# Performance work log

Hardware: AMD Instinct MI355X
Metric: run time of the kernel (lower is better)

## Reference

```python
import jax, jax.numpy as jnp
import numpy as np

B, H, W, C = 32, 56, 56, 256
RATE = 0.5


def setup_inputs() -> dict:
    key = jax.random.key(0)
    k1, k2, k3 = jax.random.split(key, 3)
    x = jax.random.normal(k1, (B, H, W, C), dtype=jnp.float32)
    # One independent spatial permutation per channel (shared across batch),
    # matching tf.random_shuffle of the [H*W, B, 1] reshaped slice.
    perm = jnp.argsort(jax.random.uniform(k2, (C, H * W)), axis=1).astype(jnp.int32)
    # Random subset of floor(rate*C) channels is jumbled (0/1 blend mask),
    # matching tf.scatter_nd over a shuffled channel index vector.
    n_sel = int(np.floor(RATE * C))
    chan_order = jax.random.permutation(k3, C)
    mask = jnp.zeros((C,), dtype=jnp.float32).at[chan_order[:n_sel]].set(1.0)
    return {"x": x, "mask": mask, "perm": perm}


def reference(x, mask, perm) -> jnp.ndarray:
    b, h, w, c = x.shape
    xf = x.reshape(b, h * w, c)                      # [B, HW, C]
    # shuffled[b, p, ch] = xf[b, perm[ch, p], ch]
    shuf = jnp.take_along_axis(xf, perm.T[None, :, :], axis=1)  # [B, HW, C]
    out = shuf * mask + xf * (1.0 - mask)            # per-channel blend
    return out.reshape(b, h, w, c)
```

## Files before the change

kernel.cpp:

```cpp
#include <hip/hip_runtime.h>

#define BATCH 32
#define HW    3136
#define NCH   256
#define CHB   8
#define THREADS 1024

__global__ __launch_bounds__(THREADS) void jumble_staged_kernel(
    const float* __restrict__ x, const float* __restrict__ mask,
    const int* __restrict__ perm, float* __restrict__ out) {
  __shared__ float lds[HW * CHB];

  const unsigned hw_bid = blockIdx.x;
  const unsigned xcd = hw_bid & 7u;
  const unsigned l = hw_bid >> 3;
  const unsigned chblk = l >> 2;
  const unsigned b = 4u * xcd + (l & 3u);
  const unsigned ch0 = chblk * CHB;

  const unsigned t = threadIdx.x;

  const float4* __restrict__ xg4 = (const float4*)(x + (size_t)b * (HW * NCH));
  for (unsigned f = t; f < HW * CHB / 4; f += THREADS) {
    const unsigned p = f >> 1, cq = f & 1u;
    const float4 v = xg4[p * (NCH / 4) + (ch0 / 4) + cq];
    const unsigned cb = cq * 4u;
    lds[(cb + 0) * HW + p] = v.x;
    lds[(cb + 1) * HW + p] = v.y;
    lds[(cb + 2) * HW + p] = v.z;
    lds[(cb + 3) * HW + p] = v.w;
  }

  const unsigned cp = t & 3u;
  const unsigned c0l = 2u * cp;
  const int* __restrict__ permA = perm + (size_t)(ch0 + c0l) * HW;
  const int* __restrict__ permB = perm + (size_t)(ch0 + c0l + 1) * HW;
  const bool m0 = mask[ch0 + c0l] != 0.0f;
  const bool m1 = mask[ch0 + c0l + 1] != 0.0f;

  __syncthreads();

  float2* __restrict__ og2 = (float2*)(out + (size_t)b * (HW * NCH) + ch0);
  for (unsigned f = t; f < HW * CHB / 2; f += THREADS) {
    const unsigned p = f >> 2;
    const int r0 = m0 ? permA[p] : (int)p;
    const int r1 = m1 ? permB[p] : (int)p;
    float2 v;
    v.x = lds[(c0l + 0) * HW + r0];
    v.y = lds[(c0l + 1) * HW + r1];
    og2[p * (NCH / 2) + cp] = v;
  }
}

extern "C" void kernel_launch(void* const* d_in, const int* in_sizes, int n_in,
                              void* d_out, int out_size, void* d_ws, size_t ws_size,
                              hipStream_t stream) {
  const float* x = (const float*)d_in[0];
  const float* mask = (const float*)d_in[1];
  const int* perm = (const int*)d_in[2];
  float* out = (float*)d_out;

  jumble_staged_kernel<<<BATCH * (NCH / CHB), THREADS, 0, stream>>>(
      x, mask, perm, out);
}
```

Measured before the change: 49.26 us.

## Software-pipeline channel units through double-buffered LDS with one block per batch slice

The grid shrinks to 256 blocks, one per batch image and 32-channel slice. Each block walks four 8-channel units, holding the next unit's global loads in registers while the current unit is staged into two LDS buffers and gathered. The aim is to overlap global-load latency with the LDS gather. Output stores also widen to 64 bytes of contiguous channels per pixel. In exchange, each thread carries many float4 registers and there are fewer blocks to hide latency across the GPU.

Result: slower. 112.3 us (+128.0%).

```diff
diff --git a/kernel.cpp b/kernel.cpp
--- a/kernel.cpp
+++ b/kernel.cpp
@@ -1,55 +1,141 @@
 #include <hip/hip_runtime.h>
 
-#define BATCH 32
-#define HW    3136
-#define NCH   256
-#define CHB   8
+#define HW      3136
+#define NCH     256
 #define THREADS 1024
+#define SLOTS   4
+#define TAIL    64
 
-__global__ __launch_bounds__(THREADS) void jumble_staged_kernel(
+__global__ __launch_bounds__(THREADS) void jumble_v5_kernel(
     const float* __restrict__ x, const float* __restrict__ mask,
     const int* __restrict__ perm, float* __restrict__ out) {
-  __shared__ float lds[HW * CHB];
+  __shared__ float bufA[4 * HW];
+  __shared__ float bufB[4 * HW];
 
-  const unsigned hw_bid = blockIdx.x;
-  const unsigned xcd = hw_bid & 7u;
-  const unsigned l = hw_bid >> 3;
-  const unsigned chblk = l >> 2;
-  const unsigned b = 4u * xcd + (l & 3u);
-  const unsigned ch0 = chblk * CHB;
-
+  const unsigned bid = blockIdx.x;
+  const unsigned cb32 = bid & 7u;
+  const unsigned b = bid >> 3;
+  const unsigned chb = cb32 * 32u;
   const unsigned t = threadIdx.x;
 
-  const float4* __restrict__ xg4 = (const float4*)(x + (size_t)b * (HW * NCH));
-  for (unsigned f = t; f < HW * CHB / 4; f += THREADS) {
-    const unsigned p = f >> 1, cq = f & 1u;
-    const float4 v = xg4[p * (NCH / 4) + (ch0 / 4) + cq];
-    const unsigned cb = cq * 4u;
-    lds[(cb + 0) * HW + p] = v.x;
-    lds[(cb + 1) * HW + p] = v.y;
-    lds[(cb + 2) * HW + p] = v.z;
-    lds[(cb + 3) * HW + p] = v.w;
+  const float* __restrict__ xb = x + (size_t)b * (HW * NCH);
+  float* __restrict__ ob = out + (size_t)b * (HW * NCH);
+
+  float4 lo[SLOTS] = {}, hi[SLOTS] = {};
+  float4 nlo[SLOTS] = {}, nhi[SLOTS] = {};
+  float4 e_lo[SLOTS], e_hi[SLOTS];
+  float4 o_lo[SLOTS], o_hi[SLOTS];
+
+#define VALID(j) ((j) < 3 || t < TAIL)
+#define PIX(j) (t + (unsigned)(j)*THREADS)
+
+#define LOAD_UNIT(dlo, dhi, ch0)                               \
+  {                                                            \
+    const float4* src = (const float4*)(xb + (ch0));           \
+    _Pragma("unroll") for (int j = 0; j < SLOTS; ++j) {        \
+      if (VALID(j)) dlo[j] = src[(size_t)PIX(j) * (NCH / 4)];  \
+    }                                                          \
+    _Pragma("unroll") for (int j = 0; j < SLOTS; ++j) {        \
+      if (VALID(j)) dhi[j] = src[(size_t)PIX(j) * (NCH / 4) + 1]; \
+    }                                                          \
   }
 
-  const unsigned cp = t & 3u;
-  const unsigned c0l = 2u * cp;
-  const int* __restrict__ permA = perm + (size_t)(ch0 + c0l) * HW;
-  const int* __restrict__ permB = perm + (size_t)(ch0 + c0l + 1) * HW;
-  const bool m0 = mask[ch0 + c0l] != 0.0f;
-  const bool m1 = mask[ch0 + c0l + 1] != 0.0f;
+#define STAGE(buf, v)                                          \
+  {                                                            \
+    _Pragma("unroll") for (int j = 0; j < SLOTS; ++j) {        \
+      if (VALID(j)) {                                          \
+        const unsigned p = PIX(j);                             \
+        buf[0 * HW + p] = v[j].x;                              \
+        buf[1 * HW + p] = v[j].y;                              \
+        buf[2 * HW + p] = v[j].z;                              \
+        buf[3 * HW + p] = v[j].w;                              \
+      }                                                        \
+    }                                                          \
+  }
 
+#define GATHER4(buf, c0, res)                                      \
+  {                                                                \
+    const int* __restrict__ pr0 = perm + (size_t)((c0) + 0) * HW;  \
+    const int* __restrict__ pr1 = perm + (size_t)((c0) + 1) * HW;  \
+    const int* __restrict__ pr2 = perm + (size_t)((c0) + 2) * HW;  \
+    const int* __restrict__ pr3 = perm + (size_t)((c0) + 3) * HW;  \
+    const bool m0 = mask[(c0) + 0] != 0.0f;                        \
+    const bool m1 = mask[(c0) + 1] != 0.0f;                        \
+    const bool m2 = mask[(c0) + 2] != 0.0f;                        \
+    const bool m3 = mask[(c0) + 3] != 0.0f;                        \
+    _Pragma("unroll") for (int j = 0; j < SLOTS; ++j) {            \
+      if (VALID(j)) {                                              \
+        const int p = (int)PIX(j);                                 \
+        const int r0 = m0 ? pr0[p] : p;                            \
+        const int r1 = m1 ? pr1[p] : p;                            \
+        const int r2 = m2 ? pr2[p] : p;                            \
+        const int r3 = m3 ? pr3[p] : p;                            \
+        res[j].x = buf[0 * HW + r0];                               \
+        res[j].y = buf[1 * HW + r1];                               \
+        res[j].z = buf[2 * HW + r2];                               \
+        res[j].w = buf[3 * HW + r3];                               \
+      }                                                            \
+    }                                                              \
+  }
+
+#define STORE16(chp)                                                 \
+  {                                                                  \
+    _Pragma("unroll") for (int j = 0; j < SLOTS; ++j) {              \
+      if (VALID(j)) {                                                \
+        float4* dst = (float4*)(ob + (size_t)PIX(j) * NCH + (chp));  \
+        dst[0] = e_lo[j];                                            \
+        dst[1] = e_hi[j];                                            \
+        dst[2] = o_lo[j];                                            \
+        dst[3] = o_hi[j];                                            \
+      }                                                              \
+    }                                                                \
+  }
+
+#define ROTATE()                                   \
+  {                                                \
+    _Pragma("unroll") for (int j = 0; j < SLOTS; ++j) { \
+      lo[j] = nlo[j];                              \
+      hi[j] = nhi[j];                              \
+    }                                              \
+  }
+
+  LOAD_UNIT(lo, hi, chb + 0u)
+
+  STAGE(bufA, lo)
   __syncthreads();
+  LOAD_UNIT(nlo, nhi, chb + 8u)
+  GATHER4(bufA, chb + 0u, e_lo)
+  STAGE(bufB, hi)
+  __syncthreads();
+  GATHER4(bufB, chb + 4u, e_hi)
 
-  float2* __restrict__ og2 = (float2*)(out + (size_t)b * (HW * NCH) + ch0);
-  for (unsigned f = t; f < HW * CHB / 2; f += THREADS) {
-    const unsigned p = f >> 2;
-    const int r0 = m0 ? permA[p] : (int)p;
-    const int r1 = m1 ? permB[p] : (int)p;
-    float2 v;
-    v.x = lds[(c0l + 0) * HW + r0];
-    v.y = lds[(c0l + 1) * HW + r1];
-    og2[p * (NCH / 2) + cp] = v;
-  }
+  ROTATE()
+  STAGE(bufA, lo)
+  __syncthreads();
+  LOAD_UNIT(nlo, nhi, chb + 16u)
+  GATHER4(bufA, chb + 8u, o_lo)
+  STAGE(bufB, hi)
+  __syncthreads();
+  GATHER4(bufB, chb + 12u, o_hi)
+  STORE16(chb + 0u)
+
+  ROTATE()
+  STAGE(bufA, lo)
+  __syncthreads();
+  LOAD_UNIT(nlo, nhi, chb + 24u)
+  GATHER4(bufA, chb + 16u, e_lo)
+  STAGE(bufB, hi)
+  __syncthreads();
+  GATHER4(bufB, chb + 20u, e_hi)
+
+  ROTATE()
+  STAGE(bufA, lo)
+  __syncthreads();
+  GATHER4(bufA, chb + 24u, o_lo)
+  STAGE(bufB, hi)
+  __syncthreads();
+  GATHER4(bufB, chb + 28u, o_hi)
+  STORE16(chb + 16u)
 }
 
 extern "C" void kernel_launch(void* const* d_in, const int* in_sizes, int n_in,
@@ -60,6 +146,5 @@
   const int* perm = (const int*)d_in[2];
   float* out = (float*)d_out;
 
-  jumble_staged_kernel<<<BATCH * (NCH / CHB), THREADS, 0, stream>>>(
-      x, mask, perm, out);
+  jumble_v5_kernel<<<256, THREADS, 0, stream>>>(x, mask, perm, out);
 }
```

## Process four batches per block with register-prefetched LDS staging and cached permutation indices

Applied to the files above, without the earlier changes.

Each block now handles one 8-channel group across four batches. The grid drops from 1024 to 256 blocks. Permutation indices are loaded once into registers, packed as two 16-bit values, and reused across the four batches, which removes the repeated perm reads. Global loads for the next batch are issued into registers while the current batch is gathered from LDS. A padded LDS row stride is meant to cut bank conflicts. In exchange the kernel uses more registers, adds extra barriers, and runs fewer blocks, which may leave the GPU with too little parallelism to hide memory latency.

After: 44.33 us, median of 2. 10.0% less time.

```diff
diff --git a/kernel.cpp b/kernel.cpp
--- a/kernel.cpp
+++ b/kernel.cpp
@@ -1,55 +1,114 @@
 #include <hip/hip_runtime.h>
 
-#define BATCH 32
-#define HW    3136
-#define NCH   256
-#define CHB   8
+#define HW      3136
+#define NCH     256
+#define LDP     (HW + 1)
 #define THREADS 1024
 
-__global__ __launch_bounds__(THREADS) void jumble_staged_kernel(
+#define SSLOT 7
+#define STAIL 128
+#define GSLOT 13
+#define GTAIL 256
+
+__global__ __launch_bounds__(THREADS) void jumble_v6_kernel(
     const float* __restrict__ x, const float* __restrict__ mask,
     const int* __restrict__ perm, float* __restrict__ out) {
-  __shared__ float lds[HW * CHB];
+  __shared__ float lds[8 * LDP];
 
-  const unsigned hw_bid = blockIdx.x;
-  const unsigned xcd = hw_bid & 7u;
-  const unsigned l = hw_bid >> 3;
-  const unsigned chblk = l >> 2;
-  const unsigned b = 4u * xcd + (l & 3u);
-  const unsigned ch0 = chblk * CHB;
-
+  const unsigned bid = blockIdx.x;
+  const unsigned xcd = bid & 7u;
+  const unsigned i = bid >> 3;
+  const unsigned chblk = xcd * 4u + (i & 3u);
+  const unsigned b0 = (i >> 2) * 4u;
+  const unsigned ch0 = chblk * 8u;
   const unsigned t = threadIdx.x;
-
-  const float4* __restrict__ xg4 = (const float4*)(x + (size_t)b * (HW * NCH));
-  for (unsigned f = t; f < HW * CHB / 4; f += THREADS) {
-    const unsigned p = f >> 1, cq = f & 1u;
-    const float4 v = xg4[p * (NCH / 4) + (ch0 / 4) + cq];
-    const unsigned cb = cq * 4u;
-    lds[(cb + 0) * HW + p] = v.x;
-    lds[(cb + 1) * HW + p] = v.y;
-    lds[(cb + 2) * HW + p] = v.z;
-    lds[(cb + 3) * HW + p] = v.w;
-  }
 
   const unsigned cp = t & 3u;
   const unsigned c0l = 2u * cp;
-  const int* __restrict__ permA = perm + (size_t)(ch0 + c0l) * HW;
-  const int* __restrict__ permB = perm + (size_t)(ch0 + c0l + 1) * HW;
-  const bool m0 = mask[ch0 + c0l] != 0.0f;
-  const bool m1 = mask[ch0 + c0l + 1] != 0.0f;
+  const unsigned gp0 = t >> 2;
 
+#define ISSUE(pf, bb)                                                      \
+  {                                                                        \
+    const float4* __restrict__ src =                                       \
+        (const float4*)(x + (size_t)(bb) * (HW * NCH)) + (ch0 / 4);        \
+    _Pragma("unroll") for (int j = 0; j < SSLOT; ++j) {                    \
+      const unsigned f = t + (unsigned)j * THREADS;                        \
+      if (j < SSLOT - 1 || t < STAIL)                                      \
+        pf[j] = src[(size_t)(f >> 1) * (NCH / 4) + (f & 1u)];              \
+    }                                                                      \
+  }
+
+#define DSWRITE(pf)                                                        \
+  {                                                                        \
+    _Pragma("unroll") for (int j = 0; j < SSLOT; ++j) {                    \
+      const unsigned f = t + (unsigned)j * THREADS;                        \
+      if (j < SSLOT - 1 || t < STAIL) {                                    \
+        const unsigned p = f >> 1, cb = (f & 1u) * 4u;                     \
+        lds[(cb + 0) * LDP + p] = pf[j].x;                                 \
+        lds[(cb + 1) * LDP + p] = pf[j].y;                                 \
+        lds[(cb + 2) * LDP + p] = pf[j].z;                                 \
+        lds[(cb + 3) * LDP + p] = pf[j].w;                                 \
+      }                                                                    \
+    }                                                                      \
+  }
+
+#define GATHER(bb)                                                         \
+  {                                                                        \
+    float* __restrict__ ob = out + (size_t)(bb) * (HW * NCH) + ch0;        \
+    _Pragma("unroll") for (int k = 0; k < GSLOT; ++k) {                    \
+      if (k < GSLOT - 1 || t < GTAIL) {                                    \
+        const unsigned p = gp0 + (unsigned)k * 256u;                       \
+        const unsigned rA = ridx[k] & 0xffffu;                             \
+        const unsigned rB = ridx[k] >> 16;                                 \
+        float2 v;                                                          \
+        v.x = lds[(c0l + 0) * LDP + rA];                                   \
+        v.y = lds[(c0l + 1) * LDP + rB];                                   \
+        ((float2*)(ob + (size_t)p * NCH))[cp] = v;                         \
+      }                                                                    \
+    }                                                                      \
+  }
+
+  float4 pf[SSLOT];
+
+  ISSUE(pf, b0 + 0)
+
+  const int* __restrict__ prA = perm + (size_t)(ch0 + c0l) * HW;
+  const int* __restrict__ prB = perm + (size_t)(ch0 + c0l + 1) * HW;
+  const bool mA = mask[ch0 + c0l] != 0.0f;
+  const bool mB = mask[ch0 + c0l + 1] != 0.0f;
+  unsigned ridx[GSLOT];
+#pragma unroll
+  for (int k = 0; k < GSLOT; ++k) {
+    if (k < GSLOT - 1 || t < GTAIL) {
+      const int p = (int)(gp0 + (unsigned)k * 256u);
+      const int rA = mA ? prA[p] : p;
+      const int rB = mB ? prB[p] : p;
+      ridx[k] = (unsigned)rA | ((unsigned)rB << 16);
+    }
+  }
+
+  DSWRITE(pf)
   __syncthreads();
 
-  float2* __restrict__ og2 = (float2*)(out + (size_t)b * (HW * NCH) + ch0);
-  for (unsigned f = t; f < HW * CHB / 2; f += THREADS) {
-    const unsigned p = f >> 2;
-    const int r0 = m0 ? permA[p] : (int)p;
-    const int r1 = m1 ? permB[p] : (int)p;
-    float2 v;
-    v.x = lds[(c0l + 0) * HW + r0];
-    v.y = lds[(c0l + 1) * HW + r1];
-    og2[p * (NCH / 2) + cp] = v;
-  }
+  ISSUE(pf, b0 + 1)
+  GATHER(b0 + 0)
+  __syncthreads();
+  DSWRITE(pf)
+  __syncthreads();
+
+  ISSUE(pf, b0 + 2)
+  GATHER(b0 + 1)
+  __syncthreads();
+  DSWRITE(pf)
+  __syncthreads();
+
+  ISSUE(pf, b0 + 3)
+  GATHER(b0 + 2)
+  __syncthreads();
+  DSWRITE(pf)
+  __syncthreads();
+
+  GATHER(b0 + 3)
 }
 
 extern "C" void kernel_launch(void* const* d_in, const int* in_sizes, int n_in,
@@ -60,6 +119,5 @@
   const int* perm = (const int*)d_in[2];
   float* out = (float*)d_out;
 
-  jumble_staged_kernel<<<BATCH * (NCH / CHB), THREADS, 0, stream>>>(
-      x, mask, perm, out);
+  jumble_v6_kernel<<<256, THREADS, 0, stream>>>(x, mask, perm, out);
 }
```
